# Performance work log

Measured on AMD Instinct MI355X. Metric: run time of the kernel, lower is better.

The kernel has to match this reference:

```python
import jax, jax.numpy as jnp
import numpy as np

N, NFEAT, NHID, K = 10000, 3000, 32, 10
ALPHA = 0.2


def setup_inputs() -> dict:
    key = jax.random.key(0)
    k1, k2, k3, k4, k5 = jax.random.split(key, 5)
    stdv = 1.0 / np.sqrt(NHID)
    x = jax.random.normal(k1, (N, NFEAT), dtype=jnp.float32)
    adj = jax.random.uniform(k2, (N, N), dtype=jnp.float32) / N  # row-stochastic-ish
    W = jax.random.uniform(k3, (NFEAT, NHID), minval=-stdv, maxval=stdv, dtype=jnp.float32)
    b = jax.random.uniform(k4, (NHID,), minval=-stdv, maxval=stdv, dtype=jnp.float32)
    mu = jax.random.normal(k5, (K, NHID), dtype=jnp.float32)
    return {"x": x, "adj": adj, "W": W, "b": b, "mu": mu}


def reference(x, adj, W, b, mu):
    # GCN layer: adj @ (x @ W) + b
    support = jnp.matmul(x, W)            # [N, NHID]
    z = jnp.matmul(adj, support) + b      # [N, NHID]
    # Student-t soft assignment (computed without materializing [N, K, NHID]):
    # ||z_i - mu_j||^2 = |z_i|^2 - 2 z_i.mu_j + |mu_j|^2
    z2 = jnp.sum(z * z, axis=1, keepdims=True)        # [N, 1]
    mu2 = jnp.sum(mu * mu, axis=1)                    # [K]
    d2 = z2 - 2.0 * jnp.matmul(z, mu.T) + mu2         # [N, K]
    q = 1.0 / (1.0 + d2 / ALPHA + 1e-08)
    q = q ** (ALPHA + 1.0) / 2.0
    q = q / jnp.sum(q, axis=1, keepdims=True)
    return z, q
```

## Files before the change

kernel.cpp:

```cpp
#include <hip/hip_runtime.h>
#include <math.h>


#define NH   32
#define SUBK 320
#define TRB  256

__device__ __forceinline__ void fma8x4(const float4* __restrict__ bs, int jg2,
                                       const float4* a0, const float4* a1,
                                       float acc[4][8])
{
#pragma unroll
    for (int u = 0; u < 2; ++u) {
#pragma unroll
        for (int t = 0; t < 4; ++t) {
            float4 b0 = bs[(u * 4 + t) * 8 + jg2];
            float4 b1 = bs[(u * 4 + t) * 8 + jg2 + 1];
#pragma unroll
            for (int m = 0; m < 4; ++m) {
                float4 am = u ? a1[m] : a0[m];
                float av = (t == 0) ? am.x : (t == 1) ? am.y
                         : (t == 2) ? am.z : am.w;
                acc[m][0] += av * b0.x;
                acc[m][1] += av * b0.y;
                acc[m][2] += av * b0.z;
                acc[m][3] += av * b0.w;
                acc[m][4] += av * b1.x;
                acc[m][5] += av * b1.y;
                acc[m][6] += av * b1.z;
                acc[m][7] += av * b1.w;
            }
        }
    }
}

__global__ __launch_bounds__(256) void gemm_stream32(
    const float* __restrict__ A,
    const float* __restrict__ B,
    float* __restrict__ outp,
    int M, int K, int CH)
{
    __shared__ float Bs[SUBK * NH];

    const int tid     = threadIdx.x;
    const int rowslot = tid >> 2;
    const int jg      = tid & 3;
    const int jg2     = jg << 1;
    const int row0    = blockIdx.x * TRB;
    const int sy      = blockIdx.y;
    const int k0      = sy * CH;
    const int kspl    = min(CH, K - k0);

    const float* ap[4];
#pragma unroll
    for (int m = 0; m < 4; ++m) {
        int r = row0 + rowslot + (m << 6);
        if (r > M - 1) r = M - 1;
        ap[m] = A + (size_t)r * K + k0;
    }

    float acc[4][8];
#pragma unroll
    for (int m = 0; m < 4; ++m)
#pragma unroll
        for (int j = 0; j < 8; ++j) acc[m][j] = 0.0f;

    for (int kb = 0; kb < kspl; kb += SUBK) {
        const int kcnt = min(SUBK, kspl - kb);

        {
            const float4* src = (const float4*)(B + (size_t)(k0 + kb) * NH);
            float4* dst = (float4*)Bs;
            for (int i = tid; i < kcnt * 8; i += 256) dst[i] = src[i];
        }
        __syncthreads();

        float4 A0[4], A1[4], B0[4], B1[4];
#pragma unroll
        for (int m = 0; m < 4; ++m) {
            A0[m] = *(const float4*)(ap[m] + kb);
            A1[m] = *(const float4*)(ap[m] + kb + 4);
        }

        int kk = 0;
        for (; kk + 16 <= kcnt; kk += 16) {
#pragma unroll
            for (int m = 0; m < 4; ++m) {
                B0[m] = *(const float4*)(ap[m] + kb + kk + 8);
                B1[m] = *(const float4*)(ap[m] + kb + kk + 12);
            }
            fma8x4(((const float4*)Bs) + kk * 8, jg2, A0, A1, acc);
            if (kk + 16 < kcnt) {
#pragma unroll
                for (int m = 0; m < 4; ++m) {
                    A0[m] = *(const float4*)(ap[m] + kb + kk + 16);
                    A1[m] = *(const float4*)(ap[m] + kb + kk + 20);
                }
            }
            fma8x4(((const float4*)Bs) + (kk + 8) * 8, jg2, B0, B1, acc);
        }
        if (kk < kcnt) {
            fma8x4(((const float4*)Bs) + kk * 8, jg2, A0, A1, acc);
        }
        __syncthreads();
    }

    float* op = outp + (size_t)sy * M * NH;
#pragma unroll
    for (int m = 0; m < 4; ++m) {
        int gr = row0 + rowslot + (m << 6);
        if (gr < M) {
            float4 v0 = make_float4(acc[m][0], acc[m][1], acc[m][2], acc[m][3]);
            float4 v1 = make_float4(acc[m][4], acc[m][5], acc[m][6], acc[m][7]);
            *(float4*)(op + (size_t)gr * NH + (jg << 3))     = v0;
            *(float4*)(op + (size_t)gr * NH + (jg << 3) + 4) = v1;
        }
    }
}

__global__ __launch_bounds__(256) void reduce_add(
    const float* __restrict__ parts,
    const float* __restrict__ bias,
    float* __restrict__ out,
    int total4, int nsplit)
{
    int i = blockIdx.x * blockDim.x + threadIdx.x;
    if (i >= total4) return;
    float4 s = make_float4(0.f, 0.f, 0.f, 0.f);
    for (int p = 0; p < nsplit; ++p) {
        float4 v = ((const float4*)parts)[(size_t)p * total4 + i];
        s.x += v.x; s.y += v.y; s.z += v.z; s.w += v.w;
    }
    if (bias) {
        float4 bv = ((const float4*)bias)[i & 7];
        s.x += bv.x; s.y += bv.y; s.z += bv.z; s.w += bv.w;
    }
    ((float4*)out)[i] = s;
}

__global__ __launch_bounds__(256) void qkern(
    const float* __restrict__ z,
    const float* __restrict__ mu,
    float* __restrict__ q,
    int N)
{
    const int tid  = threadIdx.x;
    const int lane = tid & 31;
    const int i    = blockIdx.x * 8 + (tid >> 5);
    if (i >= N) return;

    float zv = z[i * 32 + lane];
    float qm = 0.f, qsum = 0.f;
#pragma unroll
    for (int c = 0; c < 10; ++c) {
        float d = zv - mu[c * 32 + lane];
        float p = d * d;
#pragma unroll
        for (int m = 16; m >= 1; m >>= 1) p += __shfl_xor(p, m, 32);
        float t  = 1.0f + p * 5.0f + 1e-8f;
        float qc = powf(t, -1.2f) * 0.5f;
        qsum += qc;
        if (lane == c) qm = qc;
    }
    if (lane < 10) q[i * 10 + lane] = qm / qsum;
}

extern "C" void kernel_launch(void* const* d_in, const int* in_sizes, int n_in,
                              void* d_out, int out_size, void* d_ws, size_t ws_size,
                              hipStream_t stream)
{
    const float* x   = (const float*)d_in[0];
    const float* adj = (const float*)d_in[1];
    const float* W   = (const float*)d_in[2];
    const float* b   = (const float*)d_in[3];
    const float* mu  = (const float*)d_in[4];

    const int N = 10000, NFEAT = 3000;
    float* z_out = (float*)d_out;
    float* q_out = (float*)d_out + N * NH;

    const size_t need32 = (size_t)(32 + 1) * N * NH * sizeof(float);
    const int nsplit = (ws_size >= need32) ? 32 : 16;

    float* ws_part    = (float*)d_ws;
    float* ws_support = (float*)d_ws + (size_t)nsplit * N * NH;

    const int total4  = N * NH / 4;
    const int rowBlks = (N + TRB - 1) / TRB;
    const int redBlks = (total4 + 255) / 256;

    const int ch1 = ((NFEAT + nsplit - 1) / nsplit + 7) & ~7;
    const int ch2 = ((N     + nsplit - 1) / nsplit + 7) & ~7;

    gemm_stream32<<<dim3(rowBlks, nsplit), 256, 0, stream>>>(
        x, W, ws_part, N, NFEAT, ch1);
    reduce_add<<<redBlks, 256, 0, stream>>>(ws_part, nullptr, ws_support, total4, nsplit);
    gemm_stream32<<<dim3(rowBlks, nsplit), 256, 0, stream>>>(
        adj, ws_support, ws_part, N, N, ch2);
    reduce_add<<<redBlks, 256, 0, stream>>>(ws_part, b, z_out, total4, nsplit);
    qkern<<<(N + 7) / 8, 256, 0, stream>>>(z_out, mu, q_out, N);
}
```

Baseline: 812.6 us.

## Halve per-block row tile and per-thread column tile in split-K GEMM

Reshapes the thread mapping of the skinny split-K GEMM. Each thread now computes 4 rows x 4 columns instead of 4 x 8, with 8 column groups per row slot, so a 256-thread block covers 128 rows. The shared-memory K chunk is halved to 160. This doubles the row-block count and cuts register pressure, aiming for more blocks and better occupancy. In exchange, each A element loaded from global memory is now read by 8 threads instead of 4, which doubles A traffic through L1/L2 in this bandwidth-bound streaming kernel.

```diff
diff --git a/kernel.cpp b/kernel.cpp
--- a/kernel.cpp
+++ b/kernel.cpp
@@ -3,32 +3,27 @@
 
 
 #define NH   32
-#define SUBK 320
-#define TRB  256
+#define SUBK 160
+#define TRB  128
 
-__device__ __forceinline__ void fma8x4(const float4* __restrict__ bs, int jg2,
+__device__ __forceinline__ void fma4x4(const float4* __restrict__ bs, int jg,
                                        const float4* a0, const float4* a1,
-                                       float acc[4][8])
+                                       float acc[4][4])
 {
 #pragma unroll
     for (int u = 0; u < 2; ++u) {
 #pragma unroll
         for (int t = 0; t < 4; ++t) {
-            float4 b0 = bs[(u * 4 + t) * 8 + jg2];
-            float4 b1 = bs[(u * 4 + t) * 8 + jg2 + 1];
+            float4 b = bs[(u * 4 + t) * 8 + jg];
 #pragma unroll
             for (int m = 0; m < 4; ++m) {
                 float4 am = u ? a1[m] : a0[m];
                 float av = (t == 0) ? am.x : (t == 1) ? am.y
                          : (t == 2) ? am.z : am.w;
-                acc[m][0] += av * b0.x;
-                acc[m][1] += av * b0.y;
-                acc[m][2] += av * b0.z;
-                acc[m][3] += av * b0.w;
-                acc[m][4] += av * b1.x;
-                acc[m][5] += av * b1.y;
-                acc[m][6] += av * b1.z;
-                acc[m][7] += av * b1.w;
+                acc[m][0] += av * b.x;
+                acc[m][1] += av * b.y;
+                acc[m][2] += av * b.z;
+                acc[m][3] += av * b.w;
             }
         }
     }
@@ -43,9 +38,8 @@
     __shared__ float Bs[SUBK * NH];
 
     const int tid     = threadIdx.x;
-    const int rowslot = tid >> 2;
-    const int jg      = tid & 3;
-    const int jg2     = jg << 1;
+    const int rowslot = tid >> 3;
+    const int jg      = tid & 7;
     const int row0    = blockIdx.x * TRB;
     const int sy      = blockIdx.y;
     const int k0      = sy * CH;
@@ -54,16 +48,16 @@
     const float* ap[4];
 #pragma unroll
     for (int m = 0; m < 4; ++m) {
-        int r = row0 + rowslot + (m << 6);
+        int r = row0 + rowslot + (m << 5);
         if (r > M - 1) r = M - 1;
         ap[m] = A + (size_t)r * K + k0;
     }
 
-    float acc[4][8];
+    float acc[4][4];
 #pragma unroll
     for (int m = 0; m < 4; ++m)
 #pragma unroll
-        for (int j = 0; j < 8; ++j) acc[m][j] = 0.0f;
+        for (int j = 0; j < 4; ++j) acc[m][j] = 0.0f;
 
     for (int kb = 0; kb < kspl; kb += SUBK) {
         const int kcnt = min(SUBK, kspl - kb);
@@ -75,7 +69,7 @@
         }
         __syncthreads();
 
-        float4 A0[4], A1[4], B0[4], B1[4];
+        float4 A0[4], A1[4], P0[4], P1[4];
 #pragma unroll
         for (int m = 0; m < 4; ++m) {
             A0[m] = *(const float4*)(ap[m] + kb);
@@ -86,10 +80,10 @@
         for (; kk + 16 <= kcnt; kk += 16) {
 #pragma unroll
             for (int m = 0; m < 4; ++m) {
-                B0[m] = *(const float4*)(ap[m] + kb + kk + 8);
-                B1[m] = *(const float4*)(ap[m] + kb + kk + 12);
+                P0[m] = *(const float4*)(ap[m] + kb + kk + 8);
+                P1[m] = *(const float4*)(ap[m] + kb + kk + 12);
             }
-            fma8x4(((const float4*)Bs) + kk * 8, jg2, A0, A1, acc);
+            fma4x4(((const float4*)Bs) + kk * 8, jg, A0, A1, acc);
             if (kk + 16 < kcnt) {
 #pragma unroll
                 for (int m = 0; m < 4; ++m) {
@@ -97,10 +91,10 @@
                     A1[m] = *(const float4*)(ap[m] + kb + kk + 20);
                 }
             }
-            fma8x4(((const float4*)Bs) + (kk + 8) * 8, jg2, B0, B1, acc);
+            fma4x4(((const float4*)Bs) + (kk + 8) * 8, jg, P0, P1, acc);
         }
         if (kk < kcnt) {
-            fma8x4(((const float4*)Bs) + kk * 8, jg2, A0, A1, acc);
+            fma4x4(((const float4*)Bs) + kk * 8, jg, A0, A1, acc);
         }
         __syncthreads();
     }
@@ -108,12 +102,10 @@
     float* op = outp + (size_t)sy * M * NH;
 #pragma unroll
     for (int m = 0; m < 4; ++m) {
-        int gr = row0 + rowslot + (m << 6);
+        int gr = row0 + rowslot + (m << 5);
         if (gr < M) {
-            float4 v0 = make_float4(acc[m][0], acc[m][1], acc[m][2], acc[m][3]);
-            float4 v1 = make_float4(acc[m][4], acc[m][5], acc[m][6], acc[m][7]);
-            *(float4*)(op + (size_t)gr * NH + (jg << 3))     = v0;
-            *(float4*)(op + (size_t)gr * NH + (jg << 3) + 4) = v1;
+            float4 v = make_float4(acc[m][0], acc[m][1], acc[m][2], acc[m][3]);
+            *(float4*)(op + (size_t)gr * NH + (jg << 2)) = v;
         }
     }
 }
```

Measured after the change: 879.0 us. +8.2%, slower.
